# Performance work log

Measured on AMD Instinct MI355X. Metric: run time of the kernel, lower is better.

## Reference

```python
import jax, jax.numpy as jnp
import numpy as np

N = 50000      # nodes
E = 800000     # edges (avg degree 16)
IN = 128       # in_channels
OUT = 64       # out_channels (latent)
H = 2 * OUT    # hidden = 2*out_channels


def setup_inputs() -> dict:
    key = jax.random.key(0)
    ks = jax.random.split(key, 7)
    s = 0.1
    return {
        "x": jax.random.normal(ks[0], (N, IN), jnp.float32),
        "edge_index": jax.random.randint(ks[1], (2, E), 0, N, dtype=jnp.int64),
        "W1": jax.random.normal(ks[2], (IN, H), jnp.float32) * s,
        "b1": jnp.zeros((H,), jnp.float32),
        "Wmu": jax.random.normal(ks[3], (H, OUT), jnp.float32) * s,
        "bmu": jnp.zeros((OUT,), jnp.float32),
        "Wls": jax.random.normal(ks[4], (H, OUT), jnp.float32) * s,
        "bls": jnp.zeros((OUT,), jnp.float32),
        "eps": jax.random.normal(ks[5], (N, OUT), jnp.float32),
    }


def _gcn_conv(x, W, b, src, dst, dinv):
    # GCNConv: h = W x, out = D^-1/2 (A + I) D^-1/2 h + b
    h = x @ W                                   # [N, F]
    norm = (dinv[src] * dinv[dst])[:, None]     # [E, 1]
    agg = jax.ops.segment_sum(h[src] * norm, dst, num_segments=N)
    agg = agg + h * (dinv * dinv)[:, None]      # self-loop term
    return agg + b


def reference(x, edge_index, W1, b1, Wmu, bmu, Wls, bls, eps):
    src, dst = edge_index[0], edge_index[1]
    # degree with self-loops (PyG gcn_norm counts in-degree on dst/col)
    deg = jax.ops.segment_sum(jnp.ones((E,), x.dtype), dst, num_segments=N) + 1.0
    dinv = deg ** -0.5  # deg >= 1, safe

    h = jax.nn.relu(_gcn_conv(x, W1, b1, src, dst, dinv))
    mu = _gcn_conv(h, Wmu, bmu, src, dst, dinv)
    # Faithful to source bug: logstd also uses convmu weights
    logstd = _gcn_conv(h, Wmu, bmu, src, dst, dinv)
    # training-mode reparameterization with externally supplied noise
    zeta = mu + eps * jnp.exp(logstd)
    return (mu, logstd, zeta)
```

## Files before the change

### kernel.cpp

```cpp
#include <hip/hip_runtime.h>
#include <math.h>

#define N_NODES 50000
#define N_EDGES 800000
#define IN_C    128
#define H_C     128
#define OUT_C   64
#define BCAP    64
#define EPB     2048

typedef unsigned short u16;
typedef unsigned int   u32;

__device__ __forceinline__ u16 f2bf(float f) {
    u32 u; __builtin_memcpy(&u, &f, 4);
    u += 0x7FFFu + ((u >> 16) & 1u);
    return (u16)(u >> 16);
}
__device__ __forceinline__ float bflo(u32 p) { u32 u = p << 16;         float f; __builtin_memcpy(&f, &u, 4); return f; }
__device__ __forceinline__ float bfhi(u32 p) { u32 u = p & 0xFFFF0000u; float f; __builtin_memcpy(&f, &u, 4); return f; }

__global__ void k_detect_i64(const int* __restrict__ ei, int* __restrict__ flag) {
    int t = threadIdx.x;
    int nz = 0;
    for (int i = t; i < 256; i += 64)
        if (ei[2 * i + 1] != 0) nz = 1;
    unsigned long long b = __ballot(nz != 0);
    if (t == 0) *flag = (b == 0ULL) ? 1 : 0;
}

__device__ __forceinline__ int eidx(const int* __restrict__ ei, size_t pos, int mode) {
    return mode ? ei[pos << 1] : ei[pos];
}

__global__ void k_sort(const int* __restrict__ ei, const int* __restrict__ flag,
                       int* __restrict__ cursor, u16* __restrict__ sorted_src) {
    const int part  = blockIdx.x & 7;
    const int chunk = blockIdx.x >> 3;
    const int base  = chunk * EPB;
    const int m = *flag;
    for (int i = threadIdx.x; i < EPB; i += 256) {
        int e = base + i;
        if (e >= N_EDGES) break;
        int d = eidx(ei, (size_t)N_EDGES + e, m);
        if ((d & 7) != part) continue;
        int s = eidx(ei, (size_t)e, m);
        int c = atomicAdd(&cursor[d], 1);
        if (c < BCAP) sorted_src[((size_t)d << 6) + c] = (u16)s;
    }
}

__global__ void k_dinv(const int* __restrict__ cursor, float* __restrict__ dinv) {
    int i = blockIdx.x * blockDim.x + threadIdx.x;
    if (i < N_NODES) dinv[i] = rsqrtf((float)cursor[i] + 1.0f);
}

template <int C, int TROWS, bool XBF16, bool SCALE>
__launch_bounds__(256, 4)
__global__ void k_gemm(const char* __restrict__ Xb, const float* __restrict__ W,
                       const float* __restrict__ dinv, u16* __restrict__ out) {
    constexpr int ESZ   = XBF16 ? 2 : 4;
    constexpr int TILEB = TROWS * IN_C * ESZ;
    constexpr int NCH   = TILEB / 1024;
    constexpr int CPW   = NCH / 4;
    __shared__ char xs[TILEB];

    const int tid  = threadIdx.x;
    const int wv   = tid >> 6;
    const int lane = tid & 63;
    const int row0 = blockIdx.x * TROWS;
    const size_t limit = (size_t)N_NODES * IN_C * ESZ - 1024;

#pragma unroll
    for (int i = 0; i < CPW; ++i) {
        int ch = wv * CPW + i;
        size_t off = (size_t)row0 * IN_C * ESZ + (size_t)ch * 1024;
        if (off > limit) off = limit;
        __builtin_amdgcn_global_load_lds(
            (const __attribute__((address_space(1))) void*)(Xb + off + (size_t)lane * 16),
            (__attribute__((address_space(3))) void*)(xs + ch * 1024),
            16, 0, 0);
    }
    asm volatile("s_waitcnt vmcnt(0)" ::: "memory");
    __syncthreads();

    constexpr int TC  = C / 4;
    constexpr int NS  = 256 / TC;
    constexpr int RPT = TROWS / NS;
    const int c4 = (tid % TC) * 4;
    const int rs = tid / TC;

    float4 acc[RPT];
#pragma unroll
    for (int r = 0; r < RPT; ++r) acc[r] = make_float4(0.f, 0.f, 0.f, 0.f);

#pragma unroll 2
    for (int k4 = 0; k4 < IN_C / 4; ++k4) {
        float4 xv[RPT];
#pragma unroll
        for (int r = 0; r < RPT; ++r) {
            int xrow = rs + r * NS;
            if (!XBF16) {
                xv[r] = *reinterpret_cast<const float4*>(&xs[(size_t)(xrow * IN_C + k4 * 4) * 4]);
            } else {
                uint2 u = *reinterpret_cast<const uint2*>(&xs[(size_t)(xrow * IN_C + k4 * 4) * 2]);
                xv[r].x = bflo(u.x); xv[r].y = bfhi(u.x);
                xv[r].z = bflo(u.y); xv[r].w = bfhi(u.y);
            }
        }
        float4 w0 = *reinterpret_cast<const float4*>(W + (size_t)(4 * k4 + 0) * C + c4);
        float4 w1 = *reinterpret_cast<const float4*>(W + (size_t)(4 * k4 + 1) * C + c4);
        float4 w2 = *reinterpret_cast<const float4*>(W + (size_t)(4 * k4 + 2) * C + c4);
        float4 w3 = *reinterpret_cast<const float4*>(W + (size_t)(4 * k4 + 3) * C + c4);
#pragma unroll
        for (int r = 0; r < RPT; ++r) {
            acc[r].x = fmaf(xv[r].x, w0.x, acc[r].x);
            acc[r].y = fmaf(xv[r].x, w0.y, acc[r].y);
            acc[r].z = fmaf(xv[r].x, w0.z, acc[r].z);
            acc[r].w = fmaf(xv[r].x, w0.w, acc[r].w);
            acc[r].x = fmaf(xv[r].y, w1.x, acc[r].x);
            acc[r].y = fmaf(xv[r].y, w1.y, acc[r].y);
            acc[r].z = fmaf(xv[r].y, w1.z, acc[r].z);
            acc[r].w = fmaf(xv[r].y, w1.w, acc[r].w);
            acc[r].x = fmaf(xv[r].z, w2.x, acc[r].x);
            acc[r].y = fmaf(xv[r].z, w2.y, acc[r].y);
            acc[r].z = fmaf(xv[r].z, w2.z, acc[r].z);
            acc[r].w = fmaf(xv[r].z, w2.w, acc[r].w);
            acc[r].x = fmaf(xv[r].w, w3.x, acc[r].x);
            acc[r].y = fmaf(xv[r].w, w3.y, acc[r].y);
            acc[r].z = fmaf(xv[r].w, w3.z, acc[r].z);
            acc[r].w = fmaf(xv[r].w, w3.w, acc[r].w);
        }
    }

#pragma unroll
    for (int r = 0; r < RPT; ++r) {
        int row = row0 + rs + r * NS;
        if (row < N_NODES) {
            float di = SCALE ? dinv[row] : 1.0f;
            ushort4 o;
            o.x = f2bf(acc[r].x * di);
            o.y = f2bf(acc[r].y * di);
            o.z = f2bf(acc[r].z * di);
            o.w = f2bf(acc[r].w * di);
            *reinterpret_cast<ushort4*>(out + (size_t)row * C + c4) = o;
        }
    }
}

template <int C, int MODE>
__global__ void k_agg(const u16* __restrict__ sorted_src,
                      const int* __restrict__ cursor,
                      const float* __restrict__ dinv,
                      const u16* __restrict__ rows,
                      const float* __restrict__ bias,
                      const float* __restrict__ eps,
                      void* __restrict__ outbuf) {
    const int wave = threadIdx.x >> 6;
    const int lane = threadIdx.x & 63;
    const int n = blockIdx.x * 4 + wave;
    if (n >= N_NODES) return;

    int c = cursor[n]; if (c > BCAP) c = BCAP;
    const int beg = n << 6;
    const int end = beg + c;
    const float di = dinv[n];

    if (C == 128) {
        const u32* rw = reinterpret_cast<const u32*>(rows);
        const int pi = lane;
        float a0 = 0.f, a1 = 0.f, b0 = 0.f, b1 = 0.f;
        int j = beg;
        for (; j + 4 <= end; j += 4) {
            ushort4 s4 = *reinterpret_cast<const ushort4*>(sorted_src + j);
            u32 p0 = rw[(size_t)s4.x * 64 + pi];
            u32 p1 = rw[(size_t)s4.y * 64 + pi];
            u32 p2 = rw[(size_t)s4.z * 64 + pi];
            u32 p3 = rw[(size_t)s4.w * 64 + pi];
            a0 += bflo(p0) + bflo(p2);  a1 += bfhi(p0) + bfhi(p2);
            b0 += bflo(p1) + bflo(p3);  b1 += bfhi(p1) + bfhi(p3);
        }
        for (; j < end; ++j) {
            u32 p0 = rw[(size_t)sorted_src[j] * 64 + pi];
            a0 += bflo(p0); a1 += bfhi(p0);
        }
        u32 qn = rw[(size_t)n * 64 + pi];
        const int c0 = lane * 2;
        float px = fmaf(di, a0 + b0 + bflo(qn), bias[c0]);
        float py = fmaf(di, a1 + b1 + bfhi(qn), bias[c0 + 1]);
        ushort2 o;
        o.x = f2bf(di * fmaxf(px, 0.f));
        o.y = f2bf(di * fmaxf(py, 0.f));
        *reinterpret_cast<ushort2*>((u16*)outbuf + (size_t)n * 128 + c0) = o;
    } else {
        float a0 = 0.f, a1 = 0.f;
        int j = beg;
        for (; j + 4 <= end; j += 4) {
            ushort4 s4 = *reinterpret_cast<const ushort4*>(sorted_src + j);
            float f0, f1, f2, f3;
            { u32 u = (u32)rows[(size_t)s4.x * 64 + lane] << 16; __builtin_memcpy(&f0, &u, 4); }
            { u32 u = (u32)rows[(size_t)s4.y * 64 + lane] << 16; __builtin_memcpy(&f1, &u, 4); }
            { u32 u = (u32)rows[(size_t)s4.z * 64 + lane] << 16; __builtin_memcpy(&f2, &u, 4); }
            { u32 u = (u32)rows[(size_t)s4.w * 64 + lane] << 16; __builtin_memcpy(&f3, &u, 4); }
            a0 += f0 + f2;
            a1 += f1 + f3;
        }
        for (; j < end; ++j) {
            u32 u = (u32)rows[(size_t)sorted_src[j] * 64 + lane] << 16;
            float f; __builtin_memcpy(&f, &u, 4);
            a0 += f;
        }
        float pn;
        { u32 u = (u32)rows[(size_t)n * 64 + lane] << 16; __builtin_memcpy(&pn, &u, 4); }
        float* out = (float*)outbuf;
        float m = fmaf(di, a0 + a1 + pn, bias[lane]);
        const int NM = N_NODES * OUT_C;
        int i = n * 64 + lane;
        float z = fmaf(eps[i], expf(m), m);
        out[i]          = m;
        out[NM + i]     = m;
        out[2 * NM + i] = z;
    }
}

extern "C" void kernel_launch(void* const* d_in, const int* in_sizes, int n_in,
                              void* d_out, int out_size, void* d_ws, size_t ws_size,
                              hipStream_t stream) {
    const float* x   = (const float*)d_in[0];
    const int*   ei  = (const int*)d_in[1];
    const float* W1  = (const float*)d_in[2];
    const float* b1  = (const float*)d_in[3];
    const float* Wmu = (const float*)d_in[4];
    const float* bmu = (const float*)d_in[5];
    const float* eps = (const float*)d_in[8];
    float* out = (float*)d_out;

    char* p = (char*)d_ws;
    int*  flag   = (int*)p;                        p += 16;
    int*  cursor = (int*)p;                        p += ((size_t)N_NODES * 4 + 15) / 16 * 16;
    float* dinv  = (float*)p;                      p += ((size_t)N_NODES * 4 + 15) / 16 * 16;
    u16* sorted  = (u16*)p;                        p += ((size_t)N_NODES * BCAP * 2 + 15) / 16 * 16;
    u16* bufA    = (u16*)p;                        p += ((size_t)N_NODES * H_C * 2 + 15) / 16 * 16;
    u16* bufG    = (u16*)p;

    hipMemsetAsync(cursor, 0, (size_t)N_NODES * sizeof(int), stream);
    k_detect_i64<<<1, 64, 0, stream>>>(ei, flag);
    k_sort<<<8 * ((N_EDGES + EPB - 1) / EPB), 256, 0, stream>>>(ei, flag, cursor, sorted);
    k_dinv<<<(N_NODES + 255) / 256, 256, 0, stream>>>(cursor, dinv);

    k_gemm<H_C, 32, false, true><<<(N_NODES + 31) / 32, 256, 0, stream>>>(
        (const char*)x, W1, dinv, bufA);
    k_agg<H_C, 0><<<(N_NODES + 3) / 4, 256, 0, stream>>>(sorted, cursor, dinv, bufA, b1, nullptr, bufG);
    k_gemm<OUT_C, 32, true, false><<<(N_NODES + 31) / 32, 256, 0, stream>>>(
        (const char*)bufG, Wmu, nullptr, bufA);
    k_agg<OUT_C, 1><<<(N_NODES + 3) / 4, 256, 0, stream>>>(sorted, cursor, dinv, bufA, bmu, eps, out);
}
```

Measured before the change: 200.6 us.

## Store features in column-group-major layout so aggregation gathers stay cache-resident per group

The GEMM outputs are now written in a blocked layout: 16-channel groups, each holding all (padded) nodes contiguously. Aggregation blocks are interleaved so that each of the 8 partitions handles one channel group, with 8 lanes per node and 8 nodes per wave. Each gather then touches a smaller per-group working set (NPAD*32 bytes) that can stay in L2/MALL, which should cut random-access traffic. The GEMMs also stage per-wave tiles without a block barrier. The cost is more index arithmetic and narrow 4-byte gathers per lane.

Result: no change. 202.5 us (+0.9%).

```diff
diff --git a/kernel.cpp b/kernel.cpp
--- a/kernel.cpp
+++ b/kernel.cpp
@@ -2,6 +2,7 @@
 #include <math.h>
 
 #define N_NODES 50000
+#define NPAD    50048
 #define N_EDGES 800000
 #define IN_C    128
 #define H_C     128
@@ -55,65 +56,47 @@
     if (i < N_NODES) dinv[i] = rsqrtf((float)cursor[i] + 1.0f);
 }
 
-template <int C, int TROWS, bool XBF16, bool SCALE>
 __launch_bounds__(256, 4)
-__global__ void k_gemm(const char* __restrict__ Xb, const float* __restrict__ W,
-                       const float* __restrict__ dinv, u16* __restrict__ out) {
-    constexpr int ESZ   = XBF16 ? 2 : 4;
-    constexpr int TILEB = TROWS * IN_C * ESZ;
-    constexpr int NCH   = TILEB / 1024;
-    constexpr int CPW   = NCH / 4;
-    __shared__ char xs[TILEB];
-
-    const int tid  = threadIdx.x;
-    const int wv   = tid >> 6;
-    const int lane = tid & 63;
-    const int row0 = blockIdx.x * TROWS;
-    const size_t limit = (size_t)N_NODES * IN_C * ESZ - 1024;
-
-#pragma unroll
-    for (int i = 0; i < CPW; ++i) {
-        int ch = wv * CPW + i;
-        size_t off = (size_t)row0 * IN_C * ESZ + (size_t)ch * 1024;
+__global__ void k_gemm1(const float* __restrict__ X, const float* __restrict__ W,
+                        const float* __restrict__ dinv, u16* __restrict__ outq) {
+    __shared__ __align__(16) char xs[32768];
+    const int tid = threadIdx.x, wv = tid >> 6, lane = tid & 63;
+    const int row0 = blockIdx.x * 64 + wv * 16;
+    const size_t limit = (size_t)N_NODES * IN_C * 4 - 1024;
+    const char* Xb = (const char*)X;
+
+#pragma unroll
+    for (int chk = 0; chk < 8; ++chk) {
+        size_t off = (size_t)row0 * 512 + (size_t)chk * 1024;
         if (off > limit) off = limit;
         __builtin_amdgcn_global_load_lds(
             (const __attribute__((address_space(1))) void*)(Xb + off + (size_t)lane * 16),
-            (__attribute__((address_space(3))) void*)(xs + ch * 1024),
+            (__attribute__((address_space(3))) void*)(xs + wv * 8192 + chk * 1024 + lane * 16),
             16, 0, 0);
     }
     asm volatile("s_waitcnt vmcnt(0)" ::: "memory");
-    __syncthreads();
-
-    constexpr int TC  = C / 4;
-    constexpr int NS  = 256 / TC;
-    constexpr int RPT = TROWS / NS;
-    const int c4 = (tid % TC) * 4;
-    const int rs = tid / TC;
-
-    float4 acc[RPT];
-#pragma unroll
-    for (int r = 0; r < RPT; ++r) acc[r] = make_float4(0.f, 0.f, 0.f, 0.f);
+    __builtin_amdgcn_sched_barrier(0);
+
+    const int c4 = (lane & 31) * 4;
+    const int rs = lane >> 5;
+
+    float4 acc[8];
+#pragma unroll
+    for (int r = 0; r < 8; ++r) acc[r] = make_float4(0.f, 0.f, 0.f, 0.f);
 
 #pragma unroll 2
     for (int k4 = 0; k4 < IN_C / 4; ++k4) {
-        float4 xv[RPT];
-#pragma unroll
-        for (int r = 0; r < RPT; ++r) {
-            int xrow = rs + r * NS;
-            if (!XBF16) {
-                xv[r] = *reinterpret_cast<const float4*>(&xs[(size_t)(xrow * IN_C + k4 * 4) * 4]);
-            } else {
-                uint2 u = *reinterpret_cast<const uint2*>(&xs[(size_t)(xrow * IN_C + k4 * 4) * 2]);
-                xv[r].x = bflo(u.x); xv[r].y = bfhi(u.x);
-                xv[r].z = bflo(u.y); xv[r].w = bfhi(u.y);
-            }
-        }
-        float4 w0 = *reinterpret_cast<const float4*>(W + (size_t)(4 * k4 + 0) * C + c4);
-        float4 w1 = *reinterpret_cast<const float4*>(W + (size_t)(4 * k4 + 1) * C + c4);
-        float4 w2 = *reinterpret_cast<const float4*>(W + (size_t)(4 * k4 + 2) * C + c4);
-        float4 w3 = *reinterpret_cast<const float4*>(W + (size_t)(4 * k4 + 3) * C + c4);
-#pragma unroll
-        for (int r = 0; r < RPT; ++r) {
+        float4 xv[8];
+#pragma unroll
+        for (int r = 0; r < 8; ++r)
+            xv[r] = *reinterpret_cast<const float4*>(
+                &xs[wv * 8192 + (rs + r * 2) * 512 + k4 * 16]);
+        float4 w0 = *reinterpret_cast<const float4*>(W + (size_t)(4 * k4 + 0) * H_C + c4);
+        float4 w1 = *reinterpret_cast<const float4*>(W + (size_t)(4 * k4 + 1) * H_C + c4);
+        float4 w2 = *reinterpret_cast<const float4*>(W + (size_t)(4 * k4 + 2) * H_C + c4);
+        float4 w3 = *reinterpret_cast<const float4*>(W + (size_t)(4 * k4 + 3) * H_C + c4);
+#pragma unroll
+        for (int r = 0; r < 8; ++r) {
             acc[r].x = fmaf(xv[r].x, w0.x, acc[r].x);
             acc[r].y = fmaf(xv[r].x, w0.y, acc[r].y);
             acc[r].z = fmaf(xv[r].x, w0.z, acc[r].z);
@@ -134,21 +117,99 @@
     }
 
 #pragma unroll
-    for (int r = 0; r < RPT; ++r) {
-        int row = row0 + rs + r * NS;
+    for (int r = 0; r < 8; ++r) {
+        int row = row0 + rs + r * 2;
         if (row < N_NODES) {
-            float di = SCALE ? dinv[row] : 1.0f;
+            float di = dinv[row];
             ushort4 o;
             o.x = f2bf(acc[r].x * di);
             o.y = f2bf(acc[r].y * di);
             o.z = f2bf(acc[r].z * di);
             o.w = f2bf(acc[r].w * di);
-            *reinterpret_cast<ushort4*>(out + (size_t)row * C + c4) = o;
-        }
-    }
-}
-
-template <int C, int MODE>
+            *reinterpret_cast<ushort4*>(
+                outq + (size_t)(c4 >> 4) * (NPAD * 16) + (size_t)row * 16 + (c4 & 15)) = o;
+        }
+    }
+}
+
+__launch_bounds__(256, 4)
+__global__ void k_gemm2(const u16* __restrict__ gbuf, const float* __restrict__ W,
+                        u16* __restrict__ outp) {
+    __shared__ __align__(16) char xs[32768];
+    const int tid = threadIdx.x, wv = tid >> 6, lane = tid & 63;
+    const int row0 = blockIdx.x * 128 + wv * 32;
+    const char* Gb = (const char*)gbuf;
+
+#pragma unroll
+    for (int g = 0; g < 8; ++g) {
+        size_t off = (size_t)g * (NPAD * 32) + (size_t)row0 * 32;
+        __builtin_amdgcn_global_load_lds(
+            (const __attribute__((address_space(1))) void*)(Gb + off + (size_t)lane * 16),
+            (__attribute__((address_space(3))) void*)(xs + wv * 8192 + g * 1024 + lane * 16),
+            16, 0, 0);
+    }
+    asm volatile("s_waitcnt vmcnt(0)" ::: "memory");
+    __builtin_amdgcn_sched_barrier(0);
+
+    const int c4 = (lane & 15) * 4;
+    const int rs = lane >> 4;
+
+    float4 acc[8];
+#pragma unroll
+    for (int r = 0; r < 8; ++r) acc[r] = make_float4(0.f, 0.f, 0.f, 0.f);
+
+#pragma unroll 2
+    for (int k4 = 0; k4 < IN_C / 4; ++k4) {
+        float4 xv[8];
+#pragma unroll
+        for (int r = 0; r < 8; ++r) {
+            int rl = rs + r * 4;
+            uint2 u = *reinterpret_cast<const uint2*>(
+                &xs[wv * 8192 + (k4 >> 2) * 1024 + rl * 32 + (k4 & 3) * 8]);
+            xv[r].x = bflo(u.x); xv[r].y = bfhi(u.x);
+            xv[r].z = bflo(u.y); xv[r].w = bfhi(u.y);
+        }
+        float4 w0 = *reinterpret_cast<const float4*>(W + (size_t)(4 * k4 + 0) * OUT_C + c4);
+        float4 w1 = *reinterpret_cast<const float4*>(W + (size_t)(4 * k4 + 1) * OUT_C + c4);
+        float4 w2 = *reinterpret_cast<const float4*>(W + (size_t)(4 * k4 + 2) * OUT_C + c4);
+        float4 w3 = *reinterpret_cast<const float4*>(W + (size_t)(4 * k4 + 3) * OUT_C + c4);
+#pragma unroll
+        for (int r = 0; r < 8; ++r) {
+            acc[r].x = fmaf(xv[r].x, w0.x, acc[r].x);
+            acc[r].y = fmaf(xv[r].x, w0.y, acc[r].y);
+            acc[r].z = fmaf(xv[r].x, w0.z, acc[r].z);
+            acc[r].w = fmaf(xv[r].x, w0.w, acc[r].w);
+            acc[r].x = fmaf(xv[r].y, w1.x, acc[r].x);
+            acc[r].y = fmaf(xv[r].y, w1.y, acc[r].y);
+            acc[r].z = fmaf(xv[r].y, w1.z, acc[r].z);
+            acc[r].w = fmaf(xv[r].y, w1.w, acc[r].w);
+            acc[r].x = fmaf(xv[r].z, w2.x, acc[r].x);
+            acc[r].y = fmaf(xv[r].z, w2.y, acc[r].y);
+            acc[r].z = fmaf(xv[r].z, w2.z, acc[r].z);
+            acc[r].w = fmaf(xv[r].z, w2.w, acc[r].w);
+            acc[r].x = fmaf(xv[r].w, w3.x, acc[r].x);
+            acc[r].y = fmaf(xv[r].w, w3.y, acc[r].y);
+            acc[r].z = fmaf(xv[r].w, w3.z, acc[r].z);
+            acc[r].w = fmaf(xv[r].w, w3.w, acc[r].w);
+        }
+    }
+
+#pragma unroll
+    for (int r = 0; r < 8; ++r) {
+        int row = row0 + rs + r * 4;
+        if (row < N_NODES) {
+            ushort4 o;
+            o.x = f2bf(acc[r].x);
+            o.y = f2bf(acc[r].y);
+            o.z = f2bf(acc[r].z);
+            o.w = f2bf(acc[r].w);
+            *reinterpret_cast<ushort4*>(
+                outp + (size_t)(c4 >> 4) * (NPAD * 16) + (size_t)row * 16 + (c4 & 15)) = o;
+        }
+    }
+}
+
+template <int NGRP, int MODE>
 __global__ void k_agg(const u16* __restrict__ sorted_src,
                       const int* __restrict__ cursor,
                       const float* __restrict__ dinv,
@@ -156,70 +217,63 @@
                       const float* __restrict__ bias,
                       const float* __restrict__ eps,
                       void* __restrict__ outbuf) {
-    const int wave = threadIdx.x >> 6;
-    const int lane = threadIdx.x & 63;
-    const int n = blockIdx.x * 4 + wave;
-    if (n >= N_NODES) return;
-
-    int c = cursor[n]; if (c > BCAP) c = BCAP;
-    const int beg = n << 6;
-    const int end = beg + c;
-    const float di = dinv[n];
-
-    if (C == 128) {
-        const u32* rw = reinterpret_cast<const u32*>(rows);
-        const int pi = lane;
-        float a0 = 0.f, a1 = 0.f, b0 = 0.f, b1 = 0.f;
-        int j = beg;
-        for (; j + 4 <= end; j += 4) {
-            ushort4 s4 = *reinterpret_cast<const ushort4*>(sorted_src + j);
-            u32 p0 = rw[(size_t)s4.x * 64 + pi];
-            u32 p1 = rw[(size_t)s4.y * 64 + pi];
-            u32 p2 = rw[(size_t)s4.z * 64 + pi];
-            u32 p3 = rw[(size_t)s4.w * 64 + pi];
-            a0 += bflo(p0) + bflo(p2);  a1 += bfhi(p0) + bfhi(p2);
-            b0 += bflo(p1) + bflo(p3);  b1 += bfhi(p1) + bfhi(p3);
-        }
-        for (; j < end; ++j) {
-            u32 p0 = rw[(size_t)sorted_src[j] * 64 + pi];
-            a0 += bflo(p0); a1 += bfhi(p0);
-        }
-        u32 qn = rw[(size_t)n * 64 + pi];
-        const int c0 = lane * 2;
-        float px = fmaf(di, a0 + b0 + bflo(qn), bias[c0]);
-        float py = fmaf(di, a1 + b1 + bfhi(qn), bias[c0 + 1]);
-        ushort2 o;
-        o.x = f2bf(di * fmaxf(px, 0.f));
-        o.y = f2bf(di * fmaxf(py, 0.f));
-        *reinterpret_cast<ushort2*>((u16*)outbuf + (size_t)n * 128 + c0) = o;
-    } else {
-        float a0 = 0.f, a1 = 0.f;
-        int j = beg;
-        for (; j + 4 <= end; j += 4) {
-            ushort4 s4 = *reinterpret_cast<const ushort4*>(sorted_src + j);
-            float f0, f1, f2, f3;
-            { u32 u = (u32)rows[(size_t)s4.x * 64 + lane] << 16; __builtin_memcpy(&f0, &u, 4); }
-            { u32 u = (u32)rows[(size_t)s4.y * 64 + lane] << 16; __builtin_memcpy(&f1, &u, 4); }
-            { u32 u = (u32)rows[(size_t)s4.z * 64 + lane] << 16; __builtin_memcpy(&f2, &u, 4); }
-            { u32 u = (u32)rows[(size_t)s4.w * 64 + lane] << 16; __builtin_memcpy(&f3, &u, 4); }
-            a0 += f0 + f2;
-            a1 += f1 + f3;
-        }
-        for (; j < end; ++j) {
-            u32 u = (u32)rows[(size_t)sorted_src[j] * 64 + lane] << 16;
-            float f; __builtin_memcpy(&f, &u, 4);
-            a0 += f;
-        }
-        float pn;
-        { u32 u = (u32)rows[(size_t)n * 64 + lane] << 16; __builtin_memcpy(&pn, &u, 4); }
-        float* out = (float*)outbuf;
-        float m = fmaf(di, a0 + a1 + pn, bias[lane]);
+    const int part  = blockIdx.x & 7;
+    const int g     = part % NGRP;
+    const int sub   = part / NGRP;
+    const int RANGE = N_NODES / (8 / NGRP);
+    const int node0 = sub * RANGE + (blockIdx.x >> 3) * 32;
+    const int nlim  = sub * RANGE + RANGE;
+
+    const int wv = threadIdx.x >> 6, lane = threadIdx.x & 63;
+    const int cl = lane >> 3, pr = lane & 7;
+    const int n  = node0 + wv * 8 + cl;
+    const bool act = (n < nlim);
+
+    int c = act ? cursor[n] : 0;
+    if (c > BCAP) c = BCAP;
+    const float di = act ? dinv[n] : 0.f;
+
+    const u32* rw = reinterpret_cast<const u32*>(rows) + (size_t)g * (NPAD * 8);
+    const u16* bk = sorted_src + ((size_t)n << 6);
+
+    float a0 = 0.f, a1 = 0.f, b0 = 0.f, b1 = 0.f;
+    int j = 0;
+    for (; j + 4 <= c; j += 4) {
+        ushort4 s4 = *reinterpret_cast<const ushort4*>(bk + j);
+        u32 p0 = rw[(size_t)s4.x * 8 + pr];
+        u32 p1 = rw[(size_t)s4.y * 8 + pr];
+        u32 p2 = rw[(size_t)s4.z * 8 + pr];
+        u32 p3 = rw[(size_t)s4.w * 8 + pr];
+        a0 += bflo(p0) + bflo(p2);  a1 += bfhi(p0) + bfhi(p2);
+        b0 += bflo(p1) + bflo(p3);  b1 += bfhi(p1) + bfhi(p3);
+    }
+    for (; j < c; ++j) {
+        u32 p0 = rw[(size_t)bk[j] * 8 + pr];
+        a0 += bflo(p0); a1 += bfhi(p0);
+    }
+    u32 sn = rw[(size_t)n * 8 + pr];
+    const int ch = g * 16 + 2 * pr;
+    float s0 = a0 + b0 + bflo(sn);
+    float s1 = a1 + b1 + bfhi(sn);
+
+    if (MODE == 0) {
+        float px = fmaf(di, s0, bias[ch]);
+        float py = fmaf(di, s1, bias[ch + 1]);
+        u32 o = (u32)f2bf(di * fmaxf(px, 0.f)) | ((u32)f2bf(di * fmaxf(py, 0.f)) << 16);
+        if (act)
+            ((u32*)outbuf)[(size_t)g * (NPAD * 8) + (size_t)n * 8 + pr] = o;
+    } else if (act) {
+        float m0 = fmaf(di, s0, bias[ch]);
+        float m1 = fmaf(di, s1, bias[ch + 1]);
         const int NM = N_NODES * OUT_C;
-        int i = n * 64 + lane;
-        float z = fmaf(eps[i], expf(m), m);
-        out[i]          = m;
-        out[NM + i]     = m;
-        out[2 * NM + i] = z;
+        int i = n * 64 + ch;
+        float2 e = *reinterpret_cast<const float2*>(eps + i);
+        float z0 = fmaf(e.x, expf(m0), m0);
+        float z1 = fmaf(e.y, expf(m1), m1);
+        float* o = (float*)outbuf;
+        *reinterpret_cast<float2*>(o + i)          = make_float2(m0, m1);
+        *reinterpret_cast<float2*>(o + NM + i)     = make_float2(m0, m1);
+        *reinterpret_cast<float2*>(o + 2 * NM + i) = make_float2(z0, z1);
     }
 }
 
@@ -240,18 +294,19 @@
     int*  cursor = (int*)p;                        p += ((size_t)N_NODES * 4 + 15) / 16 * 16;
     float* dinv  = (float*)p;                      p += ((size_t)N_NODES * 4 + 15) / 16 * 16;
     u16* sorted  = (u16*)p;                        p += ((size_t)N_NODES * BCAP * 2 + 15) / 16 * 16;
-    u16* bufA    = (u16*)p;                        p += ((size_t)N_NODES * H_C * 2 + 15) / 16 * 16;
+    u16* bufA    = (u16*)p;                        p += (size_t)8 * NPAD * 32;
     u16* bufG    = (u16*)p;
+    u16* bufP    = bufA;
 
     hipMemsetAsync(cursor, 0, (size_t)N_NODES * sizeof(int), stream);
     k_detect_i64<<<1, 64, 0, stream>>>(ei, flag);
     k_sort<<<8 * ((N_EDGES + EPB - 1) / EPB), 256, 0, stream>>>(ei, flag, cursor, sorted);
     k_dinv<<<(N_NODES + 255) / 256, 256, 0, stream>>>(cursor, dinv);
 
-    k_gemm<H_C, 32, false, true><<<(N_NODES + 31) / 32, 256, 0, stream>>>(
-        (const char*)x, W1, dinv, bufA);
-    k_agg<H_C, 0><<<(N_NODES + 3) / 4, 256, 0, stream>>>(sorted, cursor, dinv, bufA, b1, nullptr, bufG);
-    k_gemm<OUT_C, 32, true, false><<<(N_NODES + 31) / 32, 256, 0, stream>>>(
-        (const char*)bufG, Wmu, nullptr, bufA);
-    k_agg<OUT_C, 1><<<(N_NODES + 3) / 4, 256, 0, stream>>>(sorted, cursor, dinv, bufA, bmu, eps, out);
-}
+    k_gemm1<<<(N_NODES + 63) / 64, 256, 0, stream>>>(x, W1, dinv, bufA);
+    k_agg<8, 0><<<8 * ((N_NODES + 31) / 32), 256, 0, stream>>>(
+        sorted, cursor, dinv, bufA, b1, nullptr, bufG);
+    k_gemm2<<<(N_NODES + 127) / 128, 256, 0, stream>>>(bufG, Wmu, bufP);
+    k_agg<4, 1><<<8 * ((N_NODES / 2 + 31) / 32), 256, 0, stream>>>(
+        sorted, cursor, dinv, bufP, bmu, eps, out);
+}
```
